# Performance work log

Measured on AMD Instinct MI355X. Metric: run time of the kernel, lower is better.

## Reference

```python
import jax, jax.numpy as jnp
import numpy as np

M, K, D_M = 8, 256, 128
N, D = 65536, M * D_M


def setup_inputs() -> dict:
    key = jax.random.key(0)
    kx, kc = jax.random.split(key)
    x = jax.random.normal(kx, (N, D), dtype=jnp.float32)
    codebook = jax.random.normal(kc, (M, K, D_M), dtype=jnp.float32)
    return {"x": x, "codebook": codebook, "temperature": 1}


def _distance(x, codebook):
    # x: (n, d) -> (n, m, d_m); codebook: (m, k, d_m)
    n = x.shape[0]
    m, k, d_m = codebook.shape
    xr = x.reshape(n, m, d_m)
    x2 = jnp.sum(xr * xr, axis=-1, keepdims=True)        # (n, m, 1)
    c2 = jnp.sum(codebook * codebook, axis=-1)            # (m, k)
    inter = jnp.einsum('nmd,mkd->nmk', xr, codebook)      # (n, m, k)
    return x2 + c2 - 2.0 * inter                          # (n, m, k)


def reference(x, codebook, temperature):
    # Soft-PQ (trainable path): soft assignment over codewords per subspace,
    # then reconstruct from the codebook.
    n = x.shape[0]
    m, k, d_m = codebook.shape
    distance = _distance(x, codebook)                     # (n, m, k)
    soft = jax.nn.softmax(-distance / jnp.float32(temperature), axis=-1)
    quantized = jnp.einsum('nmk,mkd->nmd', soft, codebook).reshape(n, m * d_m)
    return quantized
```

## Files before the change

### kernel.cpp

```cpp
#include <hip/hip_runtime.h>

#define LOG2E 1.4426950408889634f

typedef _Float16 half8 __attribute__((ext_vector_type(8)));
typedef float floatx16 __attribute__((ext_vector_type(16)));

__device__ __forceinline__ void g2l16(const void* g, void* l) {
  __builtin_amdgcn_global_load_lds(
      (__attribute__((address_space(1))) void*)(unsigned long long)(g),
      (__attribute__((address_space(3))) void*)(unsigned int)(unsigned long long)(l),
      16, 0, 0);
}

__global__ __launch_bounds__(128, 4) void prep_kernel(
    const float* __restrict__ cb, const int* __restrict__ tptr,
    _Float16* __restrict__ cb16, _Float16* __restrict__ cbT,
    float* __restrict__ c2s) {
  int mk = blockIdx.x;
  int m = mk >> 8, k = mk & 255;
  int d = threadIdx.x;
  float v = cb[(size_t)mk * 128 + d];
  _Float16 h = (_Float16)v;
  cb16[(size_t)mk * 128 + d] = h;
  int kp = (k & 243) | ((k & 4) << 1) | ((k & 8) >> 1);
  cbT[((size_t)m * 128 + d) * 256 + kp] = h;
  float sq = v * v;
#pragma unroll
  for (int o = 0; o < 6; ++o) sq += __shfl_xor(sq, 1 << o, 64);
  __shared__ float part[2];
  if ((threadIdx.x & 63) == 0) part[threadIdx.x >> 6] = sq;
  __syncthreads();
  if (threadIdx.x == 0) {
    float invT = 1.0f / (float)tptr[0];
    c2s[mk] = (part[0] + part[1]) * invT * LOG2E;
  }
}

__global__ __launch_bounds__(256, 2) void pq_kernel(
    const float* __restrict__ x, const int* __restrict__ tptr,
    const _Float16* __restrict__ cb16, const _Float16* __restrict__ cbT,
    const float* __restrict__ c2s, float* __restrict__ out) {
  __shared__ __align__(16) _Float16 smem[32768];
  char* sb = (char*)smem;

  const int m = blockIdx.x & 7;
  const int tile = blockIdx.x >> 3;
  const int tid = threadIdx.x;
  const int w = tid >> 6;
  const int lane = tid & 63;
  const int n2 = lane & 31;
  const int h = lane >> 5;
  const int xrow = tile * 128 + w * 32 + n2;

  const char* cbm  = (const char*)(cb16 + (size_t)m * 256 * 128);
  const char* cbtm = (const char*)(cbT  + (size_t)m * 128 * 256);

  {
    const int swz = ((tid >> 4) & 7) << 4;
#pragma unroll
    for (int i = 0; i < 16; ++i) {
      int L = (i * 256 + tid) * 16;
      g2l16(cbm + (L ^ swz), sb + L);
    }
  }

  const float* xp = x + (size_t)xrow * 1024 + m * 128 + h * 8;
  float4 xa[8], xb[8];
#pragma unroll
  for (int kc = 0; kc < 4; ++kc) {
    xa[kc] = *(const float4*)(xp + kc * 16);
    xb[kc] = *(const float4*)(xp + kc * 16 + 4);
  }

  floatx16 acc[8];
#pragma unroll
  for (int t = 0; t < 8; ++t)
#pragma unroll
    for (int i = 0; i < 16; ++i) acc[t][i] = 0.0f;

  __syncthreads();

  const int rsw = (n2 & 7) << 4;

#pragma unroll
  for (int kc = 0; kc < 8; ++kc) {
    if (kc == 2) {
#pragma unroll
      for (int k2 = 4; k2 < 8; ++k2) {
        xa[k2] = *(const float4*)(xp + k2 * 16);
        xb[k2] = *(const float4*)(xp + k2 * 16 + 4);
      }
    }
    float f[8] = {xa[kc].x, xa[kc].y, xa[kc].z, xa[kc].w,
                  xb[kc].x, xb[kc].y, xb[kc].z, xb[kc].w};
    half8 bhi, blo;
#pragma unroll
    for (int j = 0; j < 8; ++j) {
      _Float16 hi = (_Float16)f[j];
      bhi[j] = hi;
      blo[j] = (_Float16)(f[j] - (float)hi);
    }
#pragma unroll
    for (int t = 0; t < 8; ++t) {
      int addr = (((t * 32 + n2) * 256) + kc * 32 + h * 16) ^ rsw;
      half8 a = *(const half8*)(sb + addr);
      acc[t] = __builtin_amdgcn_mfma_f32_32x32x16_f16(a, bhi, acc[t], 0, 0, 0);
      acc[t] = __builtin_amdgcn_mfma_f32_32x32x16_f16(a, blo, acc[t], 0, 0, 0);
    }
  }

  __syncthreads();

  {
    const int swz2 = ((tid >> 5) & 7) << 4;
#pragma unroll
    for (int i = 0; i < 16; ++i) {
      int L = (i * 256 + tid) * 16;
      g2l16(cbtm + (L ^ swz2), sb + L);
    }
  }

  const float invT = 1.0f / (float)tptr[0];
  const float kappa = 2.0f * invT * LOG2E;
  const float4* c2p = (const float4*)(c2s + m * 256) + h;

  float mx = -3.0e38f;
#pragma unroll
  for (int t = 0; t < 8; ++t) {
    float4 cq[4];
#pragma unroll
    for (int q = 0; q < 4; ++q) cq[q] = c2p[t * 8 + q * 2];
    float cf[16] = {cq[0].x, cq[0].y, cq[0].z, cq[0].w,
                    cq[1].x, cq[1].y, cq[1].z, cq[1].w,
                    cq[2].x, cq[2].y, cq[2].z, cq[2].w,
                    cq[3].x, cq[3].y, cq[3].z, cq[3].w};
#pragma unroll
    for (int r = 0; r < 16; ++r) {
      float v = acc[t][r] * kappa - cf[r];
      acc[t][r] = v;
      mx = fmaxf(mx, v);
    }
  }
  mx = fmaxf(mx, __shfl_xor(mx, 32));

  float s = 0.0f;
#pragma unroll
  for (int t = 0; t < 8; ++t)
#pragma unroll
    for (int r = 0; r < 16; ++r) {
      float e = exp2f(acc[t][r] - mx);
      acc[t][r] = e;
      s += e;
    }
  s += __shfl_xor(s, 32);
  const float is = 1.0f / s;

  half8 p0[8], p1[8];
#pragma unroll
  for (int t = 0; t < 8; ++t) {
#pragma unroll
    for (int r = 0; r < 8; ++r) p0[t][r] = (_Float16)(acc[t][r] * is);
#pragma unroll
    for (int r = 0; r < 8; ++r) p1[t][r] = (_Float16)(acc[t][8 + r] * is);
  }

  __syncthreads();

  floatx16 acc2[4];
#pragma unroll
  for (int t = 0; t < 4; ++t)
#pragma unroll
    for (int i = 0; i < 16; ++i) acc2[t][i] = 0.0f;

#pragma unroll
  for (int kc = 0; kc < 16; ++kc) {
    half8 b = (kc & 1) ? p1[kc >> 1] : p0[kc >> 1];
#pragma unroll
    for (int dt = 0; dt < 4; ++dt) {
      int addr = (((dt * 32 + n2) * 512) + kc * 32 + h * 16) ^ rsw;
      half8 a = *(const half8*)(sb + addr);
      acc2[dt] = __builtin_amdgcn_mfma_f32_32x32x16_f16(a, b, acc2[dt], 0, 0, 0);
    }
  }

  float* op = out + (size_t)xrow * 1024 + m * 128 + h * 4;
#pragma unroll
  for (int dt = 0; dt < 4; ++dt)
#pragma unroll
    for (int q = 0; q < 4; ++q) {
      float4 v = {acc2[dt][q * 4 + 0], acc2[dt][q * 4 + 1],
                  acc2[dt][q * 4 + 2], acc2[dt][q * 4 + 3]};
      *(float4*)(op + dt * 32 + q * 8) = v;
    }
}

extern "C" void kernel_launch(void* const* d_in, const int* in_sizes, int n_in,
                              void* d_out, int out_size, void* d_ws, size_t ws_size,
                              hipStream_t stream) {
  const float* x = (const float*)d_in[0];
  const float* cb = (const float*)d_in[1];
  const int* tptr = (const int*)d_in[2];

  _Float16* cb16 = (_Float16*)d_ws;
  _Float16* cbT = (_Float16*)((char*)d_ws + 524288);
  float* c2s = (float*)((char*)d_ws + 1048576);
  float* out = (float*)d_out;

  prep_kernel<<<2048, 128, 0, stream>>>(cb, tptr, cb16, cbT, c2s);
  pq_kernel<<<4096, 256, 0, stream>>>(x, tptr, cb16, cbT, c2s, out);
}
```

Baseline: 505.6 us.

## Make PQ kernel persistent with both codebooks resident in LDS

Switches pq_kernel to 256 persistent blocks of 512 threads. Each block loads both the codebook and its transpose for one subspace into 128KB of dynamic LDS once, then loops over 8 row tiles, prefetching the next tile's x while the softmax runs. This removes the per-tile codebook reloads and the mid-kernel barrier and LDS reuse. Softmax normalisation moves to the output, scaling by 1/sum after the second MFMA. The cost is 128KB of LDS per block, which limits occupancy to one block per CU, and only 256 blocks in the grid.

```diff
diff --git a/kernel.cpp b/kernel.cpp
--- a/kernel.cpp
+++ b/kernel.cpp
@@ -36,35 +36,44 @@
   }
 }
 
-__global__ __launch_bounds__(256, 2) void pq_kernel(
+__global__ __launch_bounds__(512, 2) void pq_kernel(
     const float* __restrict__ x, const int* __restrict__ tptr,
     const _Float16* __restrict__ cb16, const _Float16* __restrict__ cbT,
     const float* __restrict__ c2s, float* __restrict__ out) {
-  __shared__ __align__(16) _Float16 smem[32768];
-  char* sb = (char*)smem;
+  extern __shared__ __align__(16) char sb[];
+  char* sb2 = sb + 65536;
 
   const int m = blockIdx.x & 7;
-  const int tile = blockIdx.x >> 3;
+  const int bt = blockIdx.x >> 3;
   const int tid = threadIdx.x;
   const int w = tid >> 6;
   const int lane = tid & 63;
   const int n2 = lane & 31;
   const int h = lane >> 5;
-  const int xrow = tile * 128 + w * 32 + n2;
-
-  const char* cbm  = (const char*)(cb16 + (size_t)m * 256 * 128);
-  const char* cbtm = (const char*)(cbT  + (size_t)m * 128 * 256);
+
+  const char* cbm  = (const char*)(cb16 + (size_t)m * 32768);
+  const char* cbtm = (const char*)(cbT  + (size_t)m * 32768);
 
   {
-    const int swz = ((tid >> 4) & 7) << 4;
-#pragma unroll
-    for (int i = 0; i < 16; ++i) {
-      int L = (i * 256 + tid) * 16;
+    const int swz  = ((tid >> 4) & 7) << 4;
+    const int swz2 = ((tid >> 5) & 7) << 4;
+#pragma unroll
+    for (int i = 0; i < 8; ++i) {
+      int L = (i * 512 + tid) * 16;
       g2l16(cbm + (L ^ swz), sb + L);
-    }
-  }
-
-  const float* xp = x + (size_t)xrow * 1024 + m * 128 + h * 8;
+      g2l16(cbtm + (L ^ swz2), sb2 + L);
+    }
+  }
+
+  const size_t row0 = (size_t)bt * 2048 + w * 32 + n2;
+  const float* xp = x + row0 * 1024 + m * 128 + h * 8;
+  float* op = out + row0 * 1024 + m * 128 + h * 4;
+
+  const float invT = 1.0f / (float)tptr[0];
+  const float kappa = 2.0f * invT * LOG2E;
+  const float4* c2p = (const float4*)(c2s + m * 256) + h;
+  const int rsw = (n2 & 7) << 4;
+
   float4 xa[8], xb[8];
 #pragma unroll
   for (int kc = 0; kc < 4; ++kc) {
@@ -72,126 +81,117 @@
     xb[kc] = *(const float4*)(xp + kc * 16 + 4);
   }
 
-  floatx16 acc[8];
-#pragma unroll
-  for (int t = 0; t < 8; ++t)
-#pragma unroll
-    for (int i = 0; i < 16; ++i) acc[t][i] = 0.0f;
-
   __syncthreads();
 
-  const int rsw = (n2 & 7) << 4;
-
-#pragma unroll
-  for (int kc = 0; kc < 8; ++kc) {
-    if (kc == 2) {
-#pragma unroll
-      for (int k2 = 4; k2 < 8; ++k2) {
-        xa[k2] = *(const float4*)(xp + k2 * 16);
-        xb[k2] = *(const float4*)(xp + k2 * 16 + 4);
-      }
-    }
-    float f[8] = {xa[kc].x, xa[kc].y, xa[kc].z, xa[kc].w,
-                  xb[kc].x, xb[kc].y, xb[kc].z, xb[kc].w};
-    half8 bhi, blo;
-#pragma unroll
-    for (int j = 0; j < 8; ++j) {
-      _Float16 hi = (_Float16)f[j];
-      bhi[j] = hi;
-      blo[j] = (_Float16)(f[j] - (float)hi);
-    }
+#pragma unroll 1
+  for (int it = 0; it < 8; ++it) {
+    floatx16 acc[8];
+#pragma unroll
+    for (int t = 0; t < 8; ++t)
+#pragma unroll
+      for (int i = 0; i < 16; ++i) acc[t][i] = 0.0f;
+
+#pragma unroll
+    for (int kc = 0; kc < 8; ++kc) {
+      if (kc == 2) {
+#pragma unroll
+        for (int k2 = 4; k2 < 8; ++k2) {
+          xa[k2] = *(const float4*)(xp + k2 * 16);
+          xb[k2] = *(const float4*)(xp + k2 * 16 + 4);
+        }
+      }
+      float f[8] = {xa[kc].x, xa[kc].y, xa[kc].z, xa[kc].w,
+                    xb[kc].x, xb[kc].y, xb[kc].z, xb[kc].w};
+      half8 bhi, blo;
+#pragma unroll
+      for (int j = 0; j < 8; ++j) {
+        _Float16 hi = (_Float16)f[j];
+        bhi[j] = hi;
+        blo[j] = (_Float16)(f[j] - (float)hi);
+      }
+#pragma unroll
+      for (int t = 0; t < 8; ++t) {
+        int addr = (((t * 32 + n2) * 256) + kc * 32 + h * 16) ^ rsw;
+        half8 a = *(const half8*)(sb + addr);
+        acc[t] = __builtin_amdgcn_mfma_f32_32x32x16_f16(a, bhi, acc[t], 0, 0, 0);
+        acc[t] = __builtin_amdgcn_mfma_f32_32x32x16_f16(a, blo, acc[t], 0, 0, 0);
+      }
+    }
+
+    const float* xpn = xp + (it < 7 ? 262144 : 0);
+#pragma unroll
+    for (int kc = 0; kc < 4; ++kc) {
+      xa[kc] = *(const float4*)(xpn + kc * 16);
+      xb[kc] = *(const float4*)(xpn + kc * 16 + 4);
+    }
+
+    float mx = -3.0e38f;
 #pragma unroll
     for (int t = 0; t < 8; ++t) {
-      int addr = (((t * 32 + n2) * 256) + kc * 32 + h * 16) ^ rsw;
-      half8 a = *(const half8*)(sb + addr);
-      acc[t] = __builtin_amdgcn_mfma_f32_32x32x16_f16(a, bhi, acc[t], 0, 0, 0);
-      acc[t] = __builtin_amdgcn_mfma_f32_32x32x16_f16(a, blo, acc[t], 0, 0, 0);
-    }
-  }
-
-  __syncthreads();
-
-  {
-    const int swz2 = ((tid >> 5) & 7) << 4;
-#pragma unroll
-    for (int i = 0; i < 16; ++i) {
-      int L = (i * 256 + tid) * 16;
-      g2l16(cbtm + (L ^ swz2), sb + L);
-    }
-  }
-
-  const float invT = 1.0f / (float)tptr[0];
-  const float kappa = 2.0f * invT * LOG2E;
-  const float4* c2p = (const float4*)(c2s + m * 256) + h;
-
-  float mx = -3.0e38f;
-#pragma unroll
-  for (int t = 0; t < 8; ++t) {
-    float4 cq[4];
-#pragma unroll
-    for (int q = 0; q < 4; ++q) cq[q] = c2p[t * 8 + q * 2];
-    float cf[16] = {cq[0].x, cq[0].y, cq[0].z, cq[0].w,
-                    cq[1].x, cq[1].y, cq[1].z, cq[1].w,
-                    cq[2].x, cq[2].y, cq[2].z, cq[2].w,
-                    cq[3].x, cq[3].y, cq[3].z, cq[3].w};
-#pragma unroll
-    for (int r = 0; r < 16; ++r) {
-      float v = acc[t][r] * kappa - cf[r];
-      acc[t][r] = v;
-      mx = fmaxf(mx, v);
-    }
-  }
-  mx = fmaxf(mx, __shfl_xor(mx, 32));
-
-  float s = 0.0f;
-#pragma unroll
-  for (int t = 0; t < 8; ++t)
-#pragma unroll
-    for (int r = 0; r < 16; ++r) {
-      float e = exp2f(acc[t][r] - mx);
-      acc[t][r] = e;
-      s += e;
-    }
-  s += __shfl_xor(s, 32);
-  const float is = 1.0f / s;
-
-  half8 p0[8], p1[8];
-#pragma unroll
-  for (int t = 0; t < 8; ++t) {
-#pragma unroll
-    for (int r = 0; r < 8; ++r) p0[t][r] = (_Float16)(acc[t][r] * is);
-#pragma unroll
-    for (int r = 0; r < 8; ++r) p1[t][r] = (_Float16)(acc[t][8 + r] * is);
-  }
-
-  __syncthreads();
-
-  floatx16 acc2[4];
-#pragma unroll
-  for (int t = 0; t < 4; ++t)
-#pragma unroll
-    for (int i = 0; i < 16; ++i) acc2[t][i] = 0.0f;
-
-#pragma unroll
-  for (int kc = 0; kc < 16; ++kc) {
-    half8 b = (kc & 1) ? p1[kc >> 1] : p0[kc >> 1];
-#pragma unroll
-    for (int dt = 0; dt < 4; ++dt) {
-      int addr = (((dt * 32 + n2) * 512) + kc * 32 + h * 16) ^ rsw;
-      half8 a = *(const half8*)(sb + addr);
-      acc2[dt] = __builtin_amdgcn_mfma_f32_32x32x16_f16(a, b, acc2[dt], 0, 0, 0);
-    }
-  }
-
-  float* op = out + (size_t)xrow * 1024 + m * 128 + h * 4;
-#pragma unroll
-  for (int dt = 0; dt < 4; ++dt)
-#pragma unroll
-    for (int q = 0; q < 4; ++q) {
-      float4 v = {acc2[dt][q * 4 + 0], acc2[dt][q * 4 + 1],
-                  acc2[dt][q * 4 + 2], acc2[dt][q * 4 + 3]};
-      *(float4*)(op + dt * 32 + q * 8) = v;
-    }
+      float4 cq0 = c2p[t * 8 + 0];
+      float4 cq1 = c2p[t * 8 + 2];
+      float4 cq2 = c2p[t * 8 + 4];
+      float4 cq3 = c2p[t * 8 + 6];
+      float cf[16] = {cq0.x, cq0.y, cq0.z, cq0.w, cq1.x, cq1.y, cq1.z, cq1.w,
+                      cq2.x, cq2.y, cq2.z, cq2.w, cq3.x, cq3.y, cq3.z, cq3.w};
+#pragma unroll
+      for (int r = 0; r < 16; ++r) {
+        float v = acc[t][r] * kappa - cf[r];
+        acc[t][r] = v;
+        mx = fmaxf(mx, v);
+      }
+    }
+    mx = fmaxf(mx, __shfl_xor(mx, 32));
+
+    float s = 0.0f;
+    half8 p0[8], p1[8];
+#pragma unroll
+    for (int t = 0; t < 8; ++t) {
+#pragma unroll
+      for (int r = 0; r < 8; ++r) {
+        float e = exp2f(acc[t][r] - mx);
+        s += e;
+        p0[t][r] = (_Float16)e;
+      }
+#pragma unroll
+      for (int r = 0; r < 8; ++r) {
+        float e = exp2f(acc[t][8 + r] - mx);
+        s += e;
+        p1[t][r] = (_Float16)e;
+      }
+    }
+    s += __shfl_xor(s, 32);
+
+    floatx16 acc2[4];
+#pragma unroll
+    for (int t = 0; t < 4; ++t)
+#pragma unroll
+      for (int i = 0; i < 16; ++i) acc2[t][i] = 0.0f;
+
+#pragma unroll
+    for (int kc = 0; kc < 16; ++kc) {
+      half8 b = (kc & 1) ? p1[kc >> 1] : p0[kc >> 1];
+#pragma unroll
+      for (int dt = 0; dt < 4; ++dt) {
+        int addr = (((dt * 32 + n2) * 512) + kc * 32 + h * 16) ^ rsw;
+        half8 a = *(const half8*)(sb2 + addr);
+        acc2[dt] = __builtin_amdgcn_mfma_f32_32x32x16_f16(a, b, acc2[dt], 0, 0, 0);
+      }
+    }
+
+    const float is = 1.0f / s;
+#pragma unroll
+    for (int dt = 0; dt < 4; ++dt)
+#pragma unroll
+      for (int q = 0; q < 4; ++q) {
+        float4 v = {acc2[dt][q * 4 + 0] * is, acc2[dt][q * 4 + 1] * is,
+                    acc2[dt][q * 4 + 2] * is, acc2[dt][q * 4 + 3] * is};
+        *(float4*)(op + dt * 32 + q * 8) = v;
+      }
+
+    xp = xpn;
+    op += (it < 7 ? 262144 : 0);
+  }
 }
 
 extern "C" void kernel_launch(void* const* d_in, const int* in_sizes, int n_in,
@@ -206,6 +206,14 @@
   float* c2s = (float*)((char*)d_ws + 1048576);
   float* out = (float*)d_out;
 
+  static int lds_attr_set = 0;
+  if (!lds_attr_set) {
+    (void)hipFuncSetAttribute((const void*)pq_kernel,
+                              hipFuncAttributeMaxDynamicSharedMemorySize,
+                              131072);
+    lds_attr_set = 1;
+  }
+
   prep_kernel<<<2048, 128, 0, stream>>>(cb, tptr, cb16, cbT, c2s);
-  pq_kernel<<<4096, 256, 0, stream>>>(x, tptr, cb16, cbT, c2s, out);
-}
+  pq_kernel<<<256, 512, 131072, stream>>>(x, tptr, cb16, cbT, c2s, out);
+}
```

New measurement: 1.158 ms. 2.29x slower.
